# Kernel tuning notes

Hardware: AMD Instinct MI355X
Metric: run time of the kernel (lower is better)

Reference implementation:

```python
import jax, jax.numpy as jnp
import numpy as np

D_MODEL = 1024
NUM_HEADS = 16
D_K = D_MODEL // NUM_HEADS


def setup_inputs() -> dict:
    key = jax.random.key(0)
    ks = jax.random.split(key, 9)
    B, T = 4, 2048
    s = 0.02
    return {
        "x": jax.random.normal(ks[0], (B, T, D_MODEL), dtype=jnp.float32),
        "wq": jax.random.normal(ks[1], (D_MODEL, D_MODEL), dtype=jnp.float32) * s,
        "bq": jax.random.normal(ks[2], (D_MODEL,), dtype=jnp.float32) * s,
        "wk": jax.random.normal(ks[3], (D_MODEL, D_MODEL), dtype=jnp.float32) * s,
        "bk": jax.random.normal(ks[4], (D_MODEL,), dtype=jnp.float32) * s,
        "wv": jax.random.normal(ks[5], (D_MODEL, D_MODEL), dtype=jnp.float32) * s,
        "bv": jax.random.normal(ks[6], (D_MODEL,), dtype=jnp.float32) * s,
        "wo": jax.random.normal(ks[7], (D_MODEL, D_MODEL), dtype=jnp.float32) * s,
        "bo": jax.random.normal(ks[8], (D_MODEL,), dtype=jnp.float32) * s,
    }


def reference(x, wq, bq, wk, bk, wv, bv, wo, bo):
    B, T, D = x.shape
    H, dk = NUM_HEADS, D_K
    # Linear projections (torch Linear: x @ W.T + b; here weights stored as [D_in, D_out])
    q = (x @ wq + bq).reshape(B, T, H, dk).transpose(0, 2, 1, 3)  # [B,H,T,dk]
    k = (x @ wk + bk).reshape(B, T, H, dk).transpose(0, 2, 1, 3)
    v = (x @ wv + bv).reshape(B, T, H, dk).transpose(0, 2, 1, 3)
    scale = 1.0 / jnp.sqrt(jnp.asarray(dk, x.dtype))
    scores = jnp.einsum('bhqd,bhkd->bhqk', q, k) * scale  # [B,H,T,T]
    causal = jnp.tril(jnp.ones((T, T), dtype=bool))
    scores = jnp.where(causal[None, None], scores, jnp.asarray(-jnp.inf, scores.dtype))
    probs = jax.nn.softmax(scores, axis=-1)
    y = jnp.einsum('bhqk,bhkd->bhqd', probs, v)  # [B,H,T,dk]
    y = y.transpose(0, 2, 1, 3).reshape(B, T, D)
    return y @ wo + bo
```

## Files before the change

### kernel.cpp

```cpp
#include <hip/hip_runtime.h>
#include <hip/hip_bf16.h>
#include <stdint.h>

typedef __attribute__((ext_vector_type(8))) short bf16x8;
typedef __attribute__((ext_vector_type(4))) float f32x4;
typedef __hip_bfloat16 bf16_t;

#define D_MODEL 1024
#define NHEADS  16
#define DK      64
#define TSEQ    2048
#define BATCH   4
#define MTOK    (BATCH*TSEQ)

#define QSCALE 0.18033688011112042f

#define FSWZ(r) ((((r) & 3)) | ((((r) >> 3) & 1) << 2))

typedef __attribute__((address_space(3))) uint32_t lds_u32;
typedef const __attribute__((address_space(1))) uint32_t glb_u32;

__device__ __forceinline__ void load_lds16(const void* g, void* l) {
    __builtin_amdgcn_global_load_lds((glb_u32*)g, (lds_u32*)l, 16, 0, 0);
}

__global__ __launch_bounds__(256) void convert_x_kernel(const float* __restrict__ x,
                                                        bf16_t* __restrict__ out, int n4) {
    int i = blockIdx.x * 256 + threadIdx.x;
    if (i >= n4) return;
    float4 v = reinterpret_cast<const float4*>(x)[i];
    union { bf16_t h[4]; uint2 u; } p;
    p.h[0] = __float2bfloat16(v.x);
    p.h[1] = __float2bfloat16(v.y);
    p.h[2] = __float2bfloat16(v.z);
    p.h[3] = __float2bfloat16(v.w);
    reinterpret_cast<uint2*>(out)[i] = p.u;
}

__global__ __launch_bounds__(256) void transpose_w_kernel(
    const float* __restrict__ w0, const float* __restrict__ w1,
    const float* __restrict__ w2, const float* __restrict__ w3,
    bf16_t* __restrict__ o0, bf16_t* __restrict__ o1,
    bf16_t* __restrict__ o2, bf16_t* __restrict__ o3) {
    const float* w = (blockIdx.z == 0) ? w0 : (blockIdx.z == 1) ? w1 : (blockIdx.z == 2) ? w2 : w3;
    bf16_t* o = (blockIdx.z == 0) ? o0 : (blockIdx.z == 1) ? o1 : (blockIdx.z == 2) ? o2 : o3;
    const float wscale = (blockIdx.z == 0) ? QSCALE : 1.0f;
    __shared__ float tile[32][33];
    int tx = threadIdx.x, ty = threadIdx.y;
    int bx = blockIdx.x * 32;
    int by = blockIdx.y * 32;
    #pragma unroll
    for (int i = 0; i < 4; ++i)
        tile[ty + i*8][tx] = w[(bx + ty + i*8) * D_MODEL + by + tx];
    __syncthreads();
    #pragma unroll
    for (int i = 0; i < 4; ++i)
        o[(by + ty + i*8) * D_MODEL + bx + tx] = __float2bfloat16(tile[tx][ty + i*8] * wscale);
}

template<int FINAL>
__global__ __launch_bounds__(256) void gemm_staged_kernel(
    const bf16_t* __restrict__ A, const bf16_t* __restrict__ BtBase,
    const float* __restrict__ bias0, const float* __restrict__ bias1,
    const float* __restrict__ bias2, void* __restrict__ Cb) {
    const int K = D_MODEL;
    const int tid = threadIdx.x;
    const int wave = tid >> 6, lane = tid & 63;
    const int wm = wave >> 1, wn = wave & 1;

    const int flat = blockIdx.x + 8 * (blockIdx.y + 64 * blockIdx.z);
    const int xcd = flat & 7;
    const int idx = flat >> 3;
    const int bx  = idx & 7;
    const int byl = (idx >> 3) & 7;
    const int z   = FINAL ? 0 : (idx >> 6);
    const int by  = xcd * 8 + byl;

    const int mt = by * 128;
    const int nt = bx * 128;
    const int m0 = mt + wm * 64;
    const int n0 = nt + wn * 64;
    const bf16_t* Bt = BtBase + (size_t)z * (D_MODEL * D_MODEL);
    const float* bias = FINAL ? bias0 : (z == 0 ? bias0 : z == 1 ? bias1 : bias2);
    const float bscale = (!FINAL && z == 0) ? QSCALE : 1.0f;
    const int lr = lane & 15, lg = lane >> 4;

    __shared__ __align__(16) bf16_t Atile[2][128 * 64];
    __shared__ __align__(16) bf16_t Btile[2][128 * 64];

    const int srow = wave * 32 + (lane >> 3);
    const int sl = (lane & 7) ^ (lane >> 3);
    const size_t asrc0 = (size_t)(mt + srow) * K + sl * 8;
    const size_t bsrc0 = (size_t)(nt + srow) * K + sl * 8;

    f32x4 acc[4][4] = {};
    int cur = 0;
    #pragma unroll
    for (int i = 0; i < 4; ++i) {
        load_lds16(A  + asrc0 + (size_t)i * 8 * K, (char*)Atile[0] + wave * 4096 + i * 1024);
        load_lds16(Bt + bsrc0 + (size_t)i * 8 * K, (char*)Btile[0] + wave * 4096 + i * 1024);
    }

    #pragma unroll 1
    for (int k0 = 0; k0 < K; k0 += 64) {
        if (k0 + 64 < K) {
            #pragma unroll
            for (int i = 0; i < 4; ++i) {
                load_lds16(A  + asrc0 + (size_t)i * 8 * K + k0 + 64,
                           (char*)Atile[cur ^ 1] + wave * 4096 + i * 1024);
                load_lds16(Bt + bsrc0 + (size_t)i * 8 * K + k0 + 64,
                           (char*)Btile[cur ^ 1] + wave * 4096 + i * 1024);
            }
            asm volatile("s_waitcnt vmcnt(8)" ::: "memory");
        } else {
            asm volatile("s_waitcnt vmcnt(0)" ::: "memory");
        }
        __builtin_amdgcn_s_barrier();
        __builtin_amdgcn_sched_barrier(0);

        #pragma unroll
        for (int kk = 0; kk < 2; ++kk) {
            bf16x8 a[4], b[4];
            #pragma unroll
            for (int mi = 0; mi < 4; ++mi) {
                const int row = wm * 64 + mi * 16 + lr;
                a[mi] = *reinterpret_cast<const bf16x8*>(
                    (const char*)Atile[cur] + row * 128 + (((kk * 4 + lg) ^ (lr & 7)) * 16));
            }
            #pragma unroll
            for (int ni = 0; ni < 4; ++ni) {
                const int row = wn * 64 + ni * 16 + lr;
                b[ni] = *reinterpret_cast<const bf16x8*>(
                    (const char*)Btile[cur] + row * 128 + (((kk * 4 + lg) ^ (lr & 7)) * 16));
            }
            #pragma unroll
            for (int mi = 0; mi < 4; ++mi)
                #pragma unroll
                for (int ni = 0; ni < 4; ++ni)
                    acc[mi][ni] = __builtin_amdgcn_mfma_f32_16x16x32_bf16(a[mi], b[ni], acc[mi][ni], 0, 0, 0);
        }
        __builtin_amdgcn_sched_barrier(0);
        __builtin_amdgcn_s_barrier();
        cur ^= 1;
    }
    #pragma unroll
    for (int mi = 0; mi < 4; ++mi) {
        #pragma unroll
        for (int ni = 0; ni < 4; ++ni) {
            const int col = n0 + ni * 16 + lr;
            const float bv = bias[col] * bscale;
            #pragma unroll
            for (int r = 0; r < 4; ++r) {
                const int row = m0 + mi * 16 + lg * 4 + r;
                const float val = acc[mi][ni][r] + bv;
                if (FINAL) {
                    reinterpret_cast<float*>(Cb)[(size_t)row * D_MODEL + col] = val;
                } else if (z <= 1) {
                    size_t idx2 = (size_t)z * (MTOK * D_MODEL) +
                        (((size_t)(row >> 11) * NHEADS + (col >> 6)) * TSEQ + (row & 2047)) * DK + (col & 63);
                    reinterpret_cast<bf16_t*>(Cb)[idx2] = __float2bfloat16(val);
                } else {
                    size_t idx2 = (size_t)2 * (MTOK * D_MODEL) +
                        (((size_t)(row >> 11) * NHEADS + (col >> 6)) * DK + (col & 63)) * TSEQ + (row & 2047);
                    reinterpret_cast<bf16_t*>(Cb)[idx2] = __float2bfloat16(val);
                }
            }
        }
    }
}

__global__ __launch_bounds__(512) void attn_kernel(
    const bf16_t* __restrict__ Q, const bf16_t* __restrict__ K,
    const bf16_t* __restrict__ Vt, bf16_t* __restrict__ Y) {
    const int qpair = blockIdx.x;
    const int bh = blockIdx.y;
    const int tid = threadIdx.x;
    const int wave = tid >> 6, lane = tid & 63;
    const int lr = lane & 15, lg = lane >> 4;

    const bf16_t* Qh = Q + (size_t)bh * TSEQ * DK;
    const bf16_t* Kh = K + (size_t)bh * TSEQ * DK;
    const bf16_t* Vh = Vt + (size_t)bh * DK * TSEQ;

    __shared__ __align__(16) char smem[2][16384];

    const int srow = tid >> 3;
    const int sslot = (tid & 7) ^ FSWZ(srow);
    const size_t koff = (size_t)srow * DK + sslot * 8;
    const size_t voff = (size_t)srow * TSEQ + sslot * 8;

    const int rbase = (lr >> 2) * 8 + (lr & 3);
    const int bcast = (lane & 48) | (lg * 4);

    #pragma unroll 1
    for (int tt = 0; tt < 2; ++tt) {
        const int j = tt ? (15 - qpair) : qpair;
        const int NT = 2 * j + 2;
        const int q0 = j * 128 + wave * 16;

        bf16x8 qf[2];
        #pragma unroll
        for (int kk = 0; kk < 2; ++kk)
            qf[kk] = *reinterpret_cast<const bf16x8*>(&Qh[(size_t)(q0 + lr) * DK + kk*32 + lg*8]);

        f32x4 o[4] = {};
        float mrun = -__builtin_inff();
        float lrun = 0.f;

        int cur = 0;
        load_lds16(Kh + koff, smem[0] + wave * 1024);
        load_lds16(Vh + voff, smem[0] + 8192 + wave * 1024);

        #pragma unroll 1
        for (int kt = 0; kt < NT; ++kt) {
            if (kt + 1 < NT) {
                load_lds16(Kh + (size_t)(kt + 1) * 64 * DK + koff, smem[cur ^ 1] + wave * 1024);
                load_lds16(Vh + (size_t)(kt + 1) * 64 + voff, smem[cur ^ 1] + 8192 + wave * 1024);
                asm volatile("s_waitcnt vmcnt(2)" ::: "memory");
            } else {
                asm volatile("s_waitcnt vmcnt(0)" ::: "memory");
            }
            __builtin_amdgcn_s_barrier();
            __builtin_amdgcn_sched_barrier(0);

            if (kt * 64 <= q0 + 15) {
                const char* kb = smem[cur];
                f32x4 s[4] = {};
                #pragma unroll
                for (int fk = 0; fk < 4; ++fk) {
                    const int krow = (fk >> 1)*32 + (fk & 1)*4 + rbase;
                    #pragma unroll
                    for (int kk = 0; kk < 2; ++kk) {
                        const bf16x8 kv = *reinterpret_cast<const bf16x8*>(
                            kb + krow*128 + (((kk*4 + lg) ^ FSWZ(krow)) * 16));
                        s[fk] = __builtin_amdgcn_mfma_f32_16x16x32_bf16(kv, qf[kk], s[fk], 0, 0, 0);
                    }
                }
                if (kt * 64 + 63 > q0) {
                    const int qrow = q0 + lr;
                    #pragma unroll
                    for (int fk = 0; fk < 4; ++fk) {
                        const int kb0 = kt*64 + (fk >> 1)*32 + lg*8 + (fk & 1)*4;
                        #pragma unroll
                        for (int r = 0; r < 4; ++r)
                            if (kb0 + r > qrow) s[fk][r] = -__builtin_inff();
                    }
                }
                float tmax = s[0][0];
                #pragma unroll
                for (int fk = 0; fk < 4; ++fk)
                    #pragma unroll
                    for (int r = 0; r < 4; ++r)
                        tmax = fmaxf(tmax, s[fk][r]);
                tmax = fmaxf(tmax, __shfl_xor(tmax, 16, 64));
                tmax = fmaxf(tmax, __shfl_xor(tmax, 32, 64));
                if (__any(tmax - mrun > 11.5f)) {
                    const float mnew = fmaxf(mrun, tmax);
                    const float alpha = exp2f(mrun - mnew);
                    mrun = mnew;
                    lrun *= alpha;
                    #pragma unroll
                    for (int r = 0; r < 4; ++r) {
                        const float ar = __shfl(alpha, bcast + r, 64);
                        #pragma unroll
                        for (int fn = 0; fn < 4; ++fn)
                            o[fn][r] *= ar;
                    }
                }
                float tsum = 0.f;
                #pragma unroll
                for (int fk = 0; fk < 4; ++fk)
                    #pragma unroll
                    for (int r = 0; r < 4; ++r) {
                        const float p = exp2f(s[fk][r] - mrun);
                        s[fk][r] = p;
                        tsum += p;
                    }
                tsum += __shfl_xor(tsum, 16, 64);
                tsum += __shfl_xor(tsum, 32, 64);
                lrun += tsum;
                union { bf16x8 v; bf16_t h[8]; } pa[2];
                #pragma unroll
                for (int c = 0; c < 2; ++c)
                    #pragma unroll
                    for (int jj = 0; jj < 8; ++jj)
                        pa[c].h[jj] = __float2bfloat16(s[2*c + (jj >> 2)][jj & 3]);
                #pragma unroll
                for (int fn = 0; fn < 4; ++fn) {
                    const int vrow = fn*16 + lr;
                    #pragma unroll
                    for (int c = 0; c < 2; ++c) {
                        const bf16x8 vv = *reinterpret_cast<const bf16x8*>(
                            kb + 8192 + vrow*128 + (((c*4 + lg) ^ FSWZ(vrow)) * 16));
                        o[fn] = __builtin_amdgcn_mfma_f32_16x16x32_bf16(pa[c].v, vv, o[fn], 0, 0, 0);
                    }
                }
            }
            __builtin_amdgcn_sched_barrier(0);
            __builtin_amdgcn_s_barrier();
            cur ^= 1;
        }

        const int b = bh >> 4, h = bh & 15;
        #pragma unroll
        for (int r = 0; r < 4; ++r) {
            const float lsum = __shfl(lrun, bcast + r, 64);
            const float inv = 1.f / lsum;
            const int t = q0 + lg*4 + r;
            #pragma unroll
            for (int fn = 0; fn < 4; ++fn)
                Y[(((size_t)b * TSEQ + t) * NHEADS + h) * DK + fn*16 + lr] =
                    __float2bfloat16(o[fn][r] * inv);
        }
    }
}

extern "C" void kernel_launch(void* const* d_in, const int* in_sizes, int n_in,
                              void* d_out, int out_size, void* d_ws, size_t ws_size,
                              hipStream_t stream) {
    const float* x  = (const float*)d_in[0];
    const float* wq = (const float*)d_in[1];
    const float* bq = (const float*)d_in[2];
    const float* wk = (const float*)d_in[3];
    const float* bk = (const float*)d_in[4];
    const float* wv = (const float*)d_in[5];
    const float* bv = (const float*)d_in[6];
    const float* wo = (const float*)d_in[7];
    const float* bo = (const float*)d_in[8];
    float* out = (float*)d_out;

    char* ws = (char*)d_ws;
    const size_t MB = 1u << 20;
    bf16_t* xb  = (bf16_t*)(ws);
    bf16_t* Yb  = (bf16_t*)(ws);
    bf16_t* wqt = (bf16_t*)(ws + 16*MB);
    bf16_t* wkt = (bf16_t*)(ws + 18*MB);
    bf16_t* wvt = (bf16_t*)(ws + 20*MB);
    bf16_t* wot = (bf16_t*)(ws + 22*MB);
    bf16_t* Qb  = (bf16_t*)(ws + 24*MB);
    bf16_t* Kb  = (bf16_t*)(ws + 40*MB);
    bf16_t* Vtb = (bf16_t*)(ws + 56*MB);

    const int n4 = (MTOK * D_MODEL) / 4;
    convert_x_kernel<<<(n4 + 255) / 256, 256, 0, stream>>>(x, xb, n4);
    transpose_w_kernel<<<dim3(32, 32, 4), dim3(32, 8), 0, stream>>>(
        wq, wk, wv, wo, wqt, wkt, wvt, wot);

    gemm_staged_kernel<0><<<dim3(D_MODEL / 128, MTOK / 128, 3), 256, 0, stream>>>(
        xb, wqt, bq, bk, bv, Qb);

    attn_kernel<<<dim3(8, BATCH * NHEADS), 512, 0, stream>>>(Qb, Kb, Vtb, Yb);

    gemm_staged_kernel<1><<<dim3(D_MODEL / 128, MTOK / 128, 1), 256, 0, stream>>>(
        Yb, wot, bo, nullptr, nullptr, out);
}
```

Baseline: 274.1 us.

## Process two 16-row query groups per wave in attention to reuse K/V fragments

Each wave now handles 32 query rows (two MFMA groups) instead of 16, so every K and V fragment read from LDS feeds two MFMAs. Each block covers 256 query rows per pass and the grid halves to 4x64 blocks. It also adds s_setprio around the MFMA sections and sets launch_bounds(512,2) as an occupancy hint. In exchange the code uses more registers per thread, launches fewer blocks (256 total), and balances work across the causal mask more coarsely.

```diff
diff --git a/kernel.cpp b/kernel.cpp
--- a/kernel.cpp
+++ b/kernel.cpp
@@ -169,7 +169,7 @@
     }
 }
 
-__global__ __launch_bounds__(512) void attn_kernel(
+__global__ __launch_bounds__(512, 2) void attn_kernel(
     const bf16_t* __restrict__ Q, const bf16_t* __restrict__ K,
     const bf16_t* __restrict__ Vt, bf16_t* __restrict__ Y) {
     const int qpair = blockIdx.x;
@@ -194,18 +194,21 @@
 
     #pragma unroll 1
     for (int tt = 0; tt < 2; ++tt) {
-        const int j = tt ? (15 - qpair) : qpair;
-        const int NT = 2 * j + 2;
-        const int q0 = j * 128 + wave * 16;
-
-        bf16x8 qf[2];
+        const int j = tt ? (7 - qpair) : qpair;
+        const int NT = 4 * j + 4;
+        const int q0a = j * 256 + wave * 32;
+
+        bf16x8 qf[2][2];
         #pragma unroll
-        for (int kk = 0; kk < 2; ++kk)
-            qf[kk] = *reinterpret_cast<const bf16x8*>(&Qh[(size_t)(q0 + lr) * DK + kk*32 + lg*8]);
-
-        f32x4 o[4] = {};
-        float mrun = -__builtin_inff();
-        float lrun = 0.f;
+        for (int g = 0; g < 2; ++g)
+            #pragma unroll
+            for (int kk = 0; kk < 2; ++kk)
+                qf[g][kk] = *reinterpret_cast<const bf16x8*>(
+                    &Qh[(size_t)(q0a + g*16 + lr) * DK + kk*32 + lg*8]);
+
+        f32x4 o[2][4] = {};
+        float mrun[2] = { -__builtin_inff(), -__builtin_inff() };
+        float lrun[2] = { 0.f, 0.f };
 
         int cur = 0;
         load_lds16(Kh + koff, smem[0] + wave * 1024);
@@ -223,9 +226,10 @@
             __builtin_amdgcn_s_barrier();
             __builtin_amdgcn_sched_barrier(0);
 
-            if (kt * 64 <= q0 + 15) {
+            if (kt * 64 <= q0a + 31) {
                 const char* kb = smem[cur];
-                f32x4 s[4] = {};
+                f32x4 s[2][4] = {};
+                __builtin_amdgcn_s_setprio(1);
                 #pragma unroll
                 for (int fk = 0; fk < 4; ++fk) {
                     const int krow = (fk >> 1)*32 + (fk & 1)*4 + rbase;
@@ -233,58 +237,83 @@
                     for (int kk = 0; kk < 2; ++kk) {
                         const bf16x8 kv = *reinterpret_cast<const bf16x8*>(
                             kb + krow*128 + (((kk*4 + lg) ^ FSWZ(krow)) * 16));
-                        s[fk] = __builtin_amdgcn_mfma_f32_16x16x32_bf16(kv, qf[kk], s[fk], 0, 0, 0);
-                    }
-                }
-                if (kt * 64 + 63 > q0) {
-                    const int qrow = q0 + lr;
-                    #pragma unroll
-                    for (int fk = 0; fk < 4; ++fk) {
-                        const int kb0 = kt*64 + (fk >> 1)*32 + lg*8 + (fk & 1)*4;
+                        #pragma unroll
+                        for (int g = 0; g < 2; ++g)
+                            s[g][fk] = __builtin_amdgcn_mfma_f32_16x16x32_bf16(kv, qf[g][kk], s[g][fk], 0, 0, 0);
+                    }
+                }
+                __builtin_amdgcn_s_setprio(0);
+                if (kt * 64 + 63 > q0a) {
+                    #pragma unroll
+                    for (int g = 0; g < 2; ++g) {
+                        const int qrow = q0a + g*16 + lr;
+                        #pragma unroll
+                        for (int fk = 0; fk < 4; ++fk) {
+                            const int kb0 = kt*64 + (fk >> 1)*32 + lg*8 + (fk & 1)*4;
+                            #pragma unroll
+                            for (int r = 0; r < 4; ++r)
+                                if (kb0 + r > qrow) s[g][fk][r] = -__builtin_inff();
+                        }
+                    }
+                }
+                float tmax[2];
+                #pragma unroll
+                for (int g = 0; g < 2; ++g) {
+                    float t = s[g][0][0];
+                    #pragma unroll
+                    for (int fk = 0; fk < 4; ++fk)
                         #pragma unroll
                         for (int r = 0; r < 4; ++r)
-                            if (kb0 + r > qrow) s[fk][r] = -__builtin_inff();
-                    }
-                }
-                float tmax = s[0][0];
-                #pragma unroll
-                for (int fk = 0; fk < 4; ++fk)
-                    #pragma unroll
-                    for (int r = 0; r < 4; ++r)
-                        tmax = fmaxf(tmax, s[fk][r]);
-                tmax = fmaxf(tmax, __shfl_xor(tmax, 16, 64));
-                tmax = fmaxf(tmax, __shfl_xor(tmax, 32, 64));
-                if (__any(tmax - mrun > 11.5f)) {
-                    const float mnew = fmaxf(mrun, tmax);
-                    const float alpha = exp2f(mrun - mnew);
-                    mrun = mnew;
-                    lrun *= alpha;
+                            t = fmaxf(t, s[g][fk][r]);
+                    t = fmaxf(t, __shfl_xor(t, 16, 64));
+                    t = fmaxf(t, __shfl_xor(t, 32, 64));
+                    tmax[g] = t;
+                }
+                const float need = fmaxf(tmax[0] - mrun[0], tmax[1] - mrun[1]);
+                if (__any(need > 11.5f)) {
+                    float alpha[2];
+                    #pragma unroll
+                    for (int g = 0; g < 2; ++g) {
+                        const float mnew = fmaxf(mrun[g], tmax[g]);
+                        alpha[g] = exp2f(mrun[g] - mnew);
+                        mrun[g] = mnew;
+                        lrun[g] *= alpha[g];
+                    }
                     #pragma unroll
                     for (int r = 0; r < 4; ++r) {
-                        const float ar = __shfl(alpha, bcast + r, 64);
-                        #pragma unroll
-                        for (int fn = 0; fn < 4; ++fn)
-                            o[fn][r] *= ar;
-                    }
-                }
-                float tsum = 0.f;
-                #pragma unroll
-                for (int fk = 0; fk < 4; ++fk)
-                    #pragma unroll
-                    for (int r = 0; r < 4; ++r) {
-                        const float p = exp2f(s[fk][r] - mrun);
-                        s[fk][r] = p;
-                        tsum += p;
-                    }
-                tsum += __shfl_xor(tsum, 16, 64);
-                tsum += __shfl_xor(tsum, 32, 64);
-                lrun += tsum;
-                union { bf16x8 v; bf16_t h[8]; } pa[2];
-                #pragma unroll
-                for (int c = 0; c < 2; ++c)
-                    #pragma unroll
-                    for (int jj = 0; jj < 8; ++jj)
-                        pa[c].h[jj] = __float2bfloat16(s[2*c + (jj >> 2)][jj & 3]);
+                        const float a0 = __shfl(alpha[0], bcast + r, 64);
+                        const float a1 = __shfl(alpha[1], bcast + r, 64);
+                        #pragma unroll
+                        for (int fn = 0; fn < 4; ++fn) {
+                            o[0][fn][r] *= a0;
+                            o[1][fn][r] *= a1;
+                        }
+                    }
+                }
+                #pragma unroll
+                for (int g = 0; g < 2; ++g) {
+                    float tsum = 0.f;
+                    #pragma unroll
+                    for (int fk = 0; fk < 4; ++fk)
+                        #pragma unroll
+                        for (int r = 0; r < 4; ++r) {
+                            const float p = exp2f(s[g][fk][r] - mrun[g]);
+                            s[g][fk][r] = p;
+                            tsum += p;
+                        }
+                    tsum += __shfl_xor(tsum, 16, 64);
+                    tsum += __shfl_xor(tsum, 32, 64);
+                    lrun[g] += tsum;
+                }
+                union { bf16x8 v; bf16_t h[8]; } pa[2][2];
+                #pragma unroll
+                for (int g = 0; g < 2; ++g)
+                    #pragma unroll
+                    for (int c = 0; c < 2; ++c)
+                        #pragma unroll
+                        for (int jj = 0; jj < 8; ++jj)
+                            pa[g][c].h[jj] = __float2bfloat16(s[g][2*c + (jj >> 2)][jj & 3]);
+                __builtin_amdgcn_s_setprio(1);
                 #pragma unroll
                 for (int fn = 0; fn < 4; ++fn) {
                     const int vrow = fn*16 + lr;
@@ -292,9 +321,12 @@
                     for (int c = 0; c < 2; ++c) {
                         const bf16x8 vv = *reinterpret_cast<const bf16x8*>(
                             kb + 8192 + vrow*128 + (((c*4 + lg) ^ FSWZ(vrow)) * 16));
-                        o[fn] = __builtin_amdgcn_mfma_f32_16x16x32_bf16(pa[c].v, vv, o[fn], 0, 0, 0);
-                    }
-                }
+                        #pragma unroll
+                        for (int g = 0; g < 2; ++g)
+                            o[g][fn] = __builtin_amdgcn_mfma_f32_16x16x32_bf16(pa[g][c].v, vv, o[g][fn], 0, 0, 0);
+                    }
+                }
+                __builtin_amdgcn_s_setprio(0);
             }
             __builtin_amdgcn_sched_barrier(0);
             __builtin_amdgcn_s_barrier();
@@ -303,15 +335,17 @@
 
         const int b = bh >> 4, h = bh & 15;
         #pragma unroll
-        for (int r = 0; r < 4; ++r) {
-            const float lsum = __shfl(lrun, bcast + r, 64);
-            const float inv = 1.f / lsum;
-            const int t = q0 + lg*4 + r;
-            #pragma unroll
-            for (int fn = 0; fn < 4; ++fn)
-                Y[(((size_t)b * TSEQ + t) * NHEADS + h) * DK + fn*16 + lr] =
-                    __float2bfloat16(o[fn][r] * inv);
-        }
+        for (int g = 0; g < 2; ++g)
+            #pragma unroll
+            for (int r = 0; r < 4; ++r) {
+                const float lsum = __shfl(lrun[g], bcast + r, 64);
+                const float inv = 1.f / lsum;
+                const int t = q0a + g*16 + lg*4 + r;
+                #pragma unroll
+                for (int fn = 0; fn < 4; ++fn)
+                    Y[(((size_t)b * TSEQ + t) * NHEADS + h) * DK + fn*16 + lr] =
+                        __float2bfloat16(o[g][fn][r] * inv);
+            }
     }
 }
 
@@ -349,7 +383,7 @@
     gemm_staged_kernel<0><<<dim3(D_MODEL / 128, MTOK / 128, 3), 256, 0, stream>>>(
         xb, wqt, bq, bk, bv, Qb);
 
-    attn_kernel<<<dim3(8, BATCH * NHEADS), 512, 0, stream>>>(Qb, Kb, Vtb, Yb);
+    attn_kernel<<<dim3(4, BATCH * NHEADS), 512, 0, stream>>>(Qb, Kb, Vtb, Yb);
 
     gemm_staged_kernel<1><<<dim3(D_MODEL / 128, MTOK / 128, 1), 256, 0, stream>>>(
         Yb, wot, bo, nullptr, nullptr, out);
```

Result: no change. 276.2 us (+0.8%).

## Restructure attention into small 64-query blocks with XCD-aware head mapping

Applied to the files above, without the earlier changes.

The attention kernel moves from 512-thread blocks that each process a pair of 128-row query tiles (balanced causal pairing) to 2048 blocks of 256 threads, each handling a single 64-row query tile. Block indices are remapped so each XCD gets a contiguous group of heads for L2 reuse of K/V, and launch bounds request 8 blocks per CU. The K/V double buffer becomes a single buffer loaded synchronously each iteration, with setprio raised around the MFMA sections. The row-sum shuffle reduction is deferred to the end. This trades the load-balancing pairing and prefetch overlap for higher occupancy and more blocks, relying on other co-resident blocks to hide the load latency.

```diff
diff --git a/kernel.cpp b/kernel.cpp
--- a/kernel.cpp
+++ b/kernel.cpp
@@ -169,149 +169,146 @@
     }
 }
 
-__global__ __launch_bounds__(512) void attn_kernel(
+__global__ __launch_bounds__(256, 8) void attn_kernel(
     const bf16_t* __restrict__ Q, const bf16_t* __restrict__ K,
     const bf16_t* __restrict__ Vt, bf16_t* __restrict__ Y) {
-    const int qpair = blockIdx.x;
-    const int bh = blockIdx.y;
+    const int flat = blockIdx.x;
+    const int xcd = flat & 7;
+    const int inner = flat >> 3;
+    const int bh = xcd * 8 + (inner & 7);
+    const int j = inner >> 3;
     const int tid = threadIdx.x;
     const int wave = tid >> 6, lane = tid & 63;
     const int lr = lane & 15, lg = lane >> 4;
+    const int q0 = j * 64 + wave * 16;
+    const int NT = j + 1;
 
     const bf16_t* Qh = Q + (size_t)bh * TSEQ * DK;
     const bf16_t* Kh = K + (size_t)bh * TSEQ * DK;
     const bf16_t* Vh = Vt + (size_t)bh * DK * TSEQ;
 
-    __shared__ __align__(16) char smem[2][16384];
-
-    const int srow = tid >> 3;
-    const int sslot = (tid & 7) ^ FSWZ(srow);
-    const size_t koff = (size_t)srow * DK + sslot * 8;
-    const size_t voff = (size_t)srow * TSEQ + sslot * 8;
+    __shared__ __align__(16) char smem[16384];
+
+    int srow[2], ssl[2];
+    #pragma unroll
+    for (int i = 0; i < 2; ++i) {
+        srow[i] = i * 32 + wave * 8 + (lane >> 3);
+        ssl[i]  = (lane & 7) ^ FSWZ(srow[i]);
+    }
 
     const int rbase = (lr >> 2) * 8 + (lr & 3);
     const int bcast = (lane & 48) | (lg * 4);
 
+    bf16x8 qf[2];
+    #pragma unroll
+    for (int kk = 0; kk < 2; ++kk)
+        qf[kk] = *reinterpret_cast<const bf16x8*>(&Qh[(size_t)(q0 + lr) * DK + kk*32 + lg*8]);
+
+    f32x4 o[4] = {};
+    float mrun = -__builtin_inff();
+    float lrun = 0.f;
+
     #pragma unroll 1
-    for (int tt = 0; tt < 2; ++tt) {
-        const int j = tt ? (15 - qpair) : qpair;
-        const int NT = 2 * j + 2;
-        const int q0 = j * 128 + wave * 16;
-
-        bf16x8 qf[2];
-        #pragma unroll
-        for (int kk = 0; kk < 2; ++kk)
-            qf[kk] = *reinterpret_cast<const bf16x8*>(&Qh[(size_t)(q0 + lr) * DK + kk*32 + lg*8]);
-
-        f32x4 o[4] = {};
-        float mrun = -__builtin_inff();
-        float lrun = 0.f;
-
-        int cur = 0;
-        load_lds16(Kh + koff, smem[0] + wave * 1024);
-        load_lds16(Vh + voff, smem[0] + 8192 + wave * 1024);
-
-        #pragma unroll 1
-        for (int kt = 0; kt < NT; ++kt) {
-            if (kt + 1 < NT) {
-                load_lds16(Kh + (size_t)(kt + 1) * 64 * DK + koff, smem[cur ^ 1] + wave * 1024);
-                load_lds16(Vh + (size_t)(kt + 1) * 64 + voff, smem[cur ^ 1] + 8192 + wave * 1024);
-                asm volatile("s_waitcnt vmcnt(2)" ::: "memory");
-            } else {
-                asm volatile("s_waitcnt vmcnt(0)" ::: "memory");
-            }
-            __builtin_amdgcn_s_barrier();
-            __builtin_amdgcn_sched_barrier(0);
-
-            if (kt * 64 <= q0 + 15) {
-                const char* kb = smem[cur];
-                f32x4 s[4] = {};
+    for (int kt = 0; kt < NT; ++kt) {
+        #pragma unroll
+        for (int i = 0; i < 2; ++i) {
+            load_lds16(Kh + (size_t)(kt*64 + srow[i]) * DK + ssl[i]*8,
+                       smem + i*4096 + wave*1024);
+            load_lds16(Vh + (size_t)srow[i] * TSEQ + kt*64 + ssl[i]*8,
+                       smem + 8192 + i*4096 + wave*1024);
+        }
+        asm volatile("s_waitcnt vmcnt(0)" ::: "memory");
+        __builtin_amdgcn_s_barrier();
+        __builtin_amdgcn_sched_barrier(0);
+
+        f32x4 s[4] = {};
+        __builtin_amdgcn_s_setprio(1);
+        #pragma unroll
+        for (int fk = 0; fk < 4; ++fk) {
+            const int krow = (fk >> 1)*32 + (fk & 1)*4 + rbase;
+            #pragma unroll
+            for (int kk = 0; kk < 2; ++kk) {
+                const bf16x8 kv = *reinterpret_cast<const bf16x8*>(
+                    smem + krow*128 + (((kk*4 + lg) ^ FSWZ(krow)) * 16));
+                s[fk] = __builtin_amdgcn_mfma_f32_16x16x32_bf16(kv, qf[kk], s[fk], 0, 0, 0);
+            }
+        }
+        __builtin_amdgcn_s_setprio(0);
+        if (kt == j) {
+            const int qrow = q0 + lr;
+            #pragma unroll
+            for (int fk = 0; fk < 4; ++fk) {
+                const int kb0 = kt*64 + (fk >> 1)*32 + lg*8 + (fk & 1)*4;
                 #pragma unroll
-                for (int fk = 0; fk < 4; ++fk) {
-                    const int krow = (fk >> 1)*32 + (fk & 1)*4 + rbase;
-                    #pragma unroll
-                    for (int kk = 0; kk < 2; ++kk) {
-                        const bf16x8 kv = *reinterpret_cast<const bf16x8*>(
-                            kb + krow*128 + (((kk*4 + lg) ^ FSWZ(krow)) * 16));
-                        s[fk] = __builtin_amdgcn_mfma_f32_16x16x32_bf16(kv, qf[kk], s[fk], 0, 0, 0);
-                    }
-                }
-                if (kt * 64 + 63 > q0) {
-                    const int qrow = q0 + lr;
-                    #pragma unroll
-                    for (int fk = 0; fk < 4; ++fk) {
-                        const int kb0 = kt*64 + (fk >> 1)*32 + lg*8 + (fk & 1)*4;
-                        #pragma unroll
-                        for (int r = 0; r < 4; ++r)
-                            if (kb0 + r > qrow) s[fk][r] = -__builtin_inff();
-                    }
-                }
-                float tmax = s[0][0];
+                for (int r = 0; r < 4; ++r)
+                    if (kb0 + r > qrow) s[fk][r] = -__builtin_inff();
+            }
+        }
+        float tmax = s[0][0];
+        #pragma unroll
+        for (int fk = 0; fk < 4; ++fk)
+            #pragma unroll
+            for (int r = 0; r < 4; ++r)
+                tmax = fmaxf(tmax, s[fk][r]);
+        tmax = fmaxf(tmax, __shfl_xor(tmax, 16, 64));
+        tmax = fmaxf(tmax, __shfl_xor(tmax, 32, 64));
+        if (__any(tmax - mrun > 11.5f)) {
+            const float mnew = fmaxf(mrun, tmax);
+            const float alpha = exp2f(mrun - mnew);
+            mrun = mnew;
+            lrun *= alpha;
+            #pragma unroll
+            for (int r = 0; r < 4; ++r) {
+                const float ar = __shfl(alpha, bcast + r, 64);
                 #pragma unroll
-                for (int fk = 0; fk < 4; ++fk)
-                    #pragma unroll
-                    for (int r = 0; r < 4; ++r)
-                        tmax = fmaxf(tmax, s[fk][r]);
-                tmax = fmaxf(tmax, __shfl_xor(tmax, 16, 64));
-                tmax = fmaxf(tmax, __shfl_xor(tmax, 32, 64));
-                if (__any(tmax - mrun > 11.5f)) {
-                    const float mnew = fmaxf(mrun, tmax);
-                    const float alpha = exp2f(mrun - mnew);
-                    mrun = mnew;
-                    lrun *= alpha;
-                    #pragma unroll
-                    for (int r = 0; r < 4; ++r) {
-                        const float ar = __shfl(alpha, bcast + r, 64);
-                        #pragma unroll
-                        for (int fn = 0; fn < 4; ++fn)
-                            o[fn][r] *= ar;
-                    }
-                }
-                float tsum = 0.f;
-                #pragma unroll
-                for (int fk = 0; fk < 4; ++fk)
-                    #pragma unroll
-                    for (int r = 0; r < 4; ++r) {
-                        const float p = exp2f(s[fk][r] - mrun);
-                        s[fk][r] = p;
-                        tsum += p;
-                    }
-                tsum += __shfl_xor(tsum, 16, 64);
-                tsum += __shfl_xor(tsum, 32, 64);
-                lrun += tsum;
-                union { bf16x8 v; bf16_t h[8]; } pa[2];
-                #pragma unroll
-                for (int c = 0; c < 2; ++c)
-                    #pragma unroll
-                    for (int jj = 0; jj < 8; ++jj)
-                        pa[c].h[jj] = __float2bfloat16(s[2*c + (jj >> 2)][jj & 3]);
-                #pragma unroll
-                for (int fn = 0; fn < 4; ++fn) {
-                    const int vrow = fn*16 + lr;
-                    #pragma unroll
-                    for (int c = 0; c < 2; ++c) {
-                        const bf16x8 vv = *reinterpret_cast<const bf16x8*>(
-                            kb + 8192 + vrow*128 + (((c*4 + lg) ^ FSWZ(vrow)) * 16));
-                        o[fn] = __builtin_amdgcn_mfma_f32_16x16x32_bf16(pa[c].v, vv, o[fn], 0, 0, 0);
-                    }
-                }
-            }
-            __builtin_amdgcn_sched_barrier(0);
-            __builtin_amdgcn_s_barrier();
-            cur ^= 1;
-        }
-
-        const int b = bh >> 4, h = bh & 15;
-        #pragma unroll
-        for (int r = 0; r < 4; ++r) {
-            const float lsum = __shfl(lrun, bcast + r, 64);
-            const float inv = 1.f / lsum;
-            const int t = q0 + lg*4 + r;
-            #pragma unroll
-            for (int fn = 0; fn < 4; ++fn)
-                Y[(((size_t)b * TSEQ + t) * NHEADS + h) * DK + fn*16 + lr] =
-                    __float2bfloat16(o[fn][r] * inv);
-        }
+                for (int fn = 0; fn < 4; ++fn)
+                    o[fn][r] *= ar;
+            }
+        }
+        float tsum = 0.f;
+        #pragma unroll
+        for (int fk = 0; fk < 4; ++fk)
+            #pragma unroll
+            for (int r = 0; r < 4; ++r) {
+                const float p = exp2f(s[fk][r] - mrun);
+                s[fk][r] = p;
+                tsum += p;
+            }
+        lrun += tsum;
+        union { bf16x8 v; bf16_t h[8]; } pa[2];
+        #pragma unroll
+        for (int c = 0; c < 2; ++c)
+            #pragma unroll
+            for (int jj = 0; jj < 8; ++jj)
+                pa[c].h[jj] = __float2bfloat16(s[2*c + (jj >> 2)][jj & 3]);
+        __builtin_amdgcn_s_setprio(1);
+        #pragma unroll
+        for (int fn = 0; fn < 4; ++fn) {
+            const int vrow = fn*16 + lr;
+            #pragma unroll
+            for (int c = 0; c < 2; ++c) {
+                const bf16x8 vv = *reinterpret_cast<const bf16x8*>(
+                    smem + 8192 + vrow*128 + (((c*4 + lg) ^ FSWZ(vrow)) * 16));
+                o[fn] = __builtin_amdgcn_mfma_f32_16x16x32_bf16(pa[c].v, vv, o[fn], 0, 0, 0);
+            }
+        }
+        __builtin_amdgcn_s_setprio(0);
+        __builtin_amdgcn_sched_barrier(0);
+        __builtin_amdgcn_s_barrier();
+    }
+
+    lrun += __shfl_xor(lrun, 16, 64);
+    lrun += __shfl_xor(lrun, 32, 64);
+    const int b = bh >> 4, h = bh & 15;
+    #pragma unroll
+    for (int r = 0; r < 4; ++r) {
+        const float lsum = __shfl(lrun, bcast + r, 64);
+        const float inv = 1.f / lsum;
+        const int t = q0 + lg*4 + r;
+        #pragma unroll
+        for (int fn = 0; fn < 4; ++fn)
+            Y[(((size_t)b * TSEQ + t) * NHEADS + h) * DK + fn*16 + lr] =
+                __float2bfloat16(o[fn][r] * inv);
     }
 }
 
@@ -349,7 +346,7 @@
     gemm_staged_kernel<0><<<dim3(D_MODEL / 128, MTOK / 128, 3), 256, 0, stream>>>(
         xb, wqt, bq, bk, bv, Qb);
 
-    attn_kernel<<<dim3(8, BATCH * NHEADS), 512, 0, stream>>>(Qb, Kb, Vtb, Yb);
+    attn_kernel<<<dim3(2048), 256, 0, stream>>>(Qb, Kb, Vtb, Yb);
 
     gemm_staged_kernel<1><<<dim3(D_MODEL / 128, MTOK / 128, 1), 256, 0, stream>>>(
         Yb, wot, bo, nullptr, nullptr, out);
```

Measured after the change: 289.9 us. 5.7% more time.
